# Kernel tuning notes

Measured on AMD Instinct MI355X. Metric: run time of the kernel, lower is better.

Reference implementation:

```python
import jax, jax.numpy as jnp
import numpy as np

B = 512              # number of graphs
NODES_PER_G = 256    # equal-size graphs (required by jagged reshape in original)
N = B * NODES_PER_G  # total nodes
DEG = 16
E = N * DEG
F = 16               # num_node_features (coords + 2-dim selected encoding)
D = 64               # embedding_dim
H = 128              # hidden_output_dim
A = 1                # actions_output_dim
MAX_LV = 3


def setup_inputs() -> dict:
    key = jax.random.key(0)
    ks = jax.random.split(key, 12)
    node_features = jax.random.normal(ks[0], (N, F), dtype=jnp.float32)
    # edges restricted to within each graph, fixed out-degree DEG
    edge_dst = jnp.repeat(jnp.arange(N, dtype=jnp.int32), DEG)
    base = (edge_dst // NODES_PER_G) * NODES_PER_G
    edge_src = base + jax.random.randint(ks[1], (E,), 0, NODES_PER_G, dtype=jnp.int32)
    seg_ids = (jnp.arange(N, dtype=jnp.int32) // NODES_PER_G)
    forbidden_mask = jax.random.bernoulli(ks[2], 0.1, (N,))
    s = 1.0 / np.sqrt(F)
    Wn = jax.random.uniform(ks[3], (F, D), jnp.float32, -s, s)
    bn = jax.random.uniform(ks[4], (D,), jnp.float32, -s, s)
    s = 1.0 / np.sqrt(D)
    Wc = jax.random.uniform(ks[5], (D, D), jnp.float32, -s, s)
    bc = jax.random.uniform(ks[6], (D,), jnp.float32, -s, s)
    s = 1.0 / np.sqrt(2 * D)
    W1 = jax.random.uniform(ks[7], (2 * D, H), jnp.float32, -s, s)
    b1 = jax.random.uniform(ks[8], (H,), jnp.float32, -s, s)
    s = 1.0 / np.sqrt(H)
    W2 = jax.random.uniform(ks[9], (H, A), jnp.float32, -s, s)
    b2 = jax.random.uniform(ks[10], (A,), jnp.float32, -s, s)
    return {"node_features": node_features, "edge_src": edge_src, "edge_dst": edge_dst,
            "seg_ids": seg_ids, "forbidden_mask": forbidden_mask,
            "Wn": Wn, "bn": bn, "Wc": Wc, "bc": bc,
            "W1": W1, "b1": b1, "W2": W2, "b2": b2}


def reference(node_features, edge_src, edge_dst, seg_ids, forbidden_mask,
              Wn, bn, Wc, bc, W1, b1, W2, b2):
    # --- structure2vec mean-field (EmbedMeanField, output_dim=0, max_lv=3) ---
    input_msg = node_features @ Wn + bn            # [N, D]
    h = jax.nn.relu(input_msg)
    for _ in range(MAX_LV):
        pooled = jax.ops.segment_sum(h[edge_src], edge_dst, num_segments=N)  # adjacency spmm
        h = jax.nn.relu(pooled @ Wc + bc + input_msg)
    graph_embed = jax.nn.relu(jax.ops.segment_sum(h, seg_ids, num_segments=B))  # [B, D]
    # --- actions is None: repeat graph embed per node, concat, small MLP ---
    rep = graph_embed[seg_ids]                     # rep_global_embed
    embed_s_a = jnp.concatenate([h, rep], axis=1)  # [N, 2D]
    raw_pred = jax.nn.relu(embed_s_a @ W1 + b1) @ W2 + b2  # [N, A]
    # --- greedy action select with forbidden-action masking + jagged topk ---
    q = raw_pred.reshape(-1)                       # A == 1
    q = jnp.where(forbidden_mask, jnp.float32(np.finfo(np.float32).min), q)
    jag = q.reshape(B, NODES_PER_G)
    values = jnp.max(jag, axis=1, keepdims=True)
    indices = jnp.argmax(jag, axis=1, keepdims=True)
    return indices, raw_pred, values
```

## Files before the change

### kernel.cpp

```cpp
#include <hip/hip_runtime.h>

#define NB 512
#define NPG 256
#define NTOT (NB * NPG)
#define NEGMIN -3.4028234663852886e38f

#define OFF_WNT 0
#define OFF_WCT 1024
#define OFF_W1AT 5120
#define OFF_W1BT 13312
#define OFF_BNC 21504
#define WS_FLOATS 21568

__global__ __launch_bounds__(256) void prep_kernel(
    const float* __restrict__ Wn, const float* __restrict__ bn,
    const float* __restrict__ Wc, const float* __restrict__ bc,
    const float* __restrict__ W1, float* __restrict__ ws)
{
    int i = blockIdx.x * 256 + threadIdx.x;
    if (i < 1024) {
        int d = i >> 4, k = i & 15;
        ws[OFF_WNT + i] = Wn[k * 64 + d];
    } else if (i < 5120) {
        int j = i - 1024; int d = j >> 6, k = j & 63;
        ws[OFF_WCT + j] = Wc[k * 64 + d];
    } else if (i < 13312) {
        int j = i - 5120; int r = j >> 6, k = j & 63;
        ws[OFF_W1AT + j] = W1[k * 128 + r];
    } else if (i < 21504) {
        int j = i - 13312; int r = j >> 6, k = j & 63;
        ws[OFF_W1BT + j] = W1[(64 + k) * 128 + r];
    } else if (i < WS_FLOATS) {
        int d = i - OFF_BNC;
        ws[OFF_BNC + d] = bn[d] + bc[d];
    }
}

__global__ __launch_bounds__(256, 2) void gdqn_kernel(
    const float* __restrict__ nfg, const int* __restrict__ esrcg,
    const int* __restrict__ fmask, const float* __restrict__ ws,
    const float* __restrict__ bn, const float* __restrict__ b1,
    const float* __restrict__ W2, const float* __restrict__ b2,
    float* __restrict__ out)
{
    extern __shared__ float smem[];
    float* hsh  = smem;
    float* part = smem + 16384;
    float* gesh = smem + 16640;
    float* rpsh = smem + 16704;
    float* redv = smem + 16832;
    int*   redi = (int*)(smem + 16836);

    const int g = blockIdx.x, t = threadIdx.x;
    const int node = (g << 8) + t;
    const int swt = t & 7;
    float* myrow = hsh + (t << 6);

    const float* WnT  = ws + OFF_WNT;
    const float* WcT  = ws + OFF_WCT;
    const float* W1aT = ws + OFF_W1AT;
    const float* bnc  = ws + OFF_BNC;

    float nf[16];
    {
        const float4* p = (const float4*)(nfg + node * 16);
        float4 a = p[0], b = p[1], c = p[2], d = p[3];
        nf[0]=a.x; nf[1]=a.y; nf[2]=a.z; nf[3]=a.w;
        nf[4]=b.x; nf[5]=b.y; nf[6]=b.z; nf[7]=b.w;
        nf[8]=c.x; nf[9]=c.y; nf[10]=c.z; nf[11]=c.w;
        nf[12]=d.x; nf[13]=d.y; nf[14]=d.z; nf[15]=d.w;
    }
    int es[16];
    {
        const int4* p = (const int4*)(esrcg + node * 16);
        int4 a = p[0], b = p[1], c = p[2], d = p[3];
        es[0]=a.x&255; es[1]=a.y&255; es[2]=a.z&255; es[3]=a.w&255;
        es[4]=b.x&255; es[5]=b.y&255; es[6]=b.z&255; es[7]=b.w&255;
        es[8]=c.x&255; es[9]=c.y&255; es[10]=c.z&255; es[11]=c.w&255;
        es[12]=d.x&255; es[13]=d.y&255; es[14]=d.z&255; es[15]=d.w&255;
    }

    for (int c = 0; c < 16; ++c) {
        float s4[4];
        #pragma unroll
        for (int q = 0; q < 4; ++q) {
            int d = 4 * c + q;
            float s = bn[d];
            #pragma unroll
            for (int k = 0; k < 16; ++k) s = fmaf(nf[k], WnT[d * 16 + k], s);
            s4[q] = fmaxf(s, 0.0f);
        }
        ((float4*)myrow)[c ^ swt] = make_float4(s4[0], s4[1], s4[2], s4[3]);
    }
    __syncthreads();

    for (int lv = 0; lv < 3; ++lv) {
        float pooled[64];
        #pragma unroll
        for (int k = 0; k < 64; ++k) pooled[k] = 0.0f;
        #pragma unroll
        for (int j = 0; j < 16; ++j) {
            int s = es[j];
            const float4* row = (const float4*)(hsh + (s << 6));
            int sw = s & 7;
            #pragma unroll
            for (int c = 0; c < 16; ++c) {
                float4 v = row[c ^ sw];
                pooled[4*c+0] += v.x; pooled[4*c+1] += v.y;
                pooled[4*c+2] += v.z; pooled[4*c+3] += v.w;
            }
        }
        __syncthreads();

        for (int c = 0; c < 16; ++c) {
            float s4[4];
            #pragma unroll
            for (int q = 0; q < 4; ++q) {
                int d = 4 * c + q;
                float s = bnc[d];
                #pragma unroll
                for (int k = 0; k < 16; ++k) s = fmaf(nf[k], WnT[d * 16 + k], s);
                const float* wr = WcT + d * 64;
                #pragma unroll
                for (int k = 0; k < 64; ++k) s = fmaf(pooled[k], wr[k], s);
                s4[q] = fmaxf(s, 0.0f);
            }
            ((float4*)myrow)[c ^ swt] = make_float4(s4[0], s4[1], s4[2], s4[3]);
        }
        __syncthreads();
    }

    {
        int col = t & 63, v0 = (t >> 6) << 6;
        float s = 0.0f;
        for (int v = 0; v < 64; ++v) {
            int vv = v0 + v;
            s += hsh[(vv << 6) + ((((col >> 2) ^ (vv & 7)) << 2) | (col & 3))];
        }
        part[t] = s;
    }
    __syncthreads();
    if (t < 64) {
        float s = part[t] + part[t + 64] + part[t + 128] + part[t + 192];
        gesh[t] = fmaxf(s, 0.0f);
    }
    __syncthreads();
    if (t < 128) {
        float s = b1[t];
        const float4* wr = (const float4*)(ws + OFF_W1BT + t * 64);
        #pragma unroll
        for (int c = 0; c < 16; ++c) {
            float4 w = wr[c];
            s = fmaf(gesh[4*c+0], w.x, s);
            s = fmaf(gesh[4*c+1], w.y, s);
            s = fmaf(gesh[4*c+2], w.z, s);
            s = fmaf(gesh[4*c+3], w.w, s);
        }
        rpsh[t] = s;
    }

    float h[64];
    #pragma unroll
    for (int c = 0; c < 16; ++c) {
        float4 v = ((const float4*)myrow)[c ^ swt];
        h[4*c+0] = v.x; h[4*c+1] = v.y; h[4*c+2] = v.z; h[4*c+3] = v.w;
    }
    __syncthreads();

    float raw = b2[0];
    for (int j = 0; j < 128; ++j) {
        float z = rpsh[j];
        const float* wr = W1aT + j * 64;
        #pragma unroll
        for (int k = 0; k < 64; ++k) z = fmaf(h[k], wr[k], z);
        raw = fmaf(fmaxf(z, 0.0f), W2[j], raw);
    }
    out[512 + node] = raw;

    float q = fmask[node] ? NEGMIN : raw;
    int idx = t;
    #pragma unroll
    for (int off = 32; off >= 1; off >>= 1) {
        float ov = __shfl_down(q, off, 64);
        int oi  = __shfl_down(idx, off, 64);
        if (ov > q || (ov == q && oi < idx)) { q = ov; idx = oi; }
    }
    if ((t & 63) == 0) { redv[t >> 6] = q; redi[t >> 6] = idx; }
    __syncthreads();
    if (t == 0) {
        float bv = redv[0]; int bi = redi[0];
        #pragma unroll
        for (int w = 1; w < 4; ++w) {
            float v = redv[w]; int iw = redi[w];
            if (v > bv || (v == bv && iw < bi)) { bv = v; bi = iw; }
        }
        out[g] = (float)bi;
        out[512 + NTOT + g] = bv;
    }
}

extern "C" void kernel_launch(void* const* d_in, const int* in_sizes, int n_in,
                              void* d_out, int out_size, void* d_ws, size_t ws_size,
                              hipStream_t stream)
{
    const float* nfg   = (const float*)d_in[0];
    const int*   esrc  = (const int*)d_in[1];
    const int*   fmask = (const int*)d_in[4];
    const float* Wn = (const float*)d_in[5];
    const float* bn = (const float*)d_in[6];
    const float* Wc = (const float*)d_in[7];
    const float* bc = (const float*)d_in[8];
    const float* W1 = (const float*)d_in[9];
    const float* b1 = (const float*)d_in[10];
    const float* W2 = (const float*)d_in[11];
    const float* b2 = (const float*)d_in[12];
    float* out = (float*)d_out;
    float* ws  = (float*)d_ws;

    prep_kernel<<<(WS_FLOATS + 255) / 256, 256, 0, stream>>>(Wn, bn, Wc, bc, W1, ws);

    size_t shmem = 16840 * sizeof(float);
    hipFuncSetAttribute((const void*)gdqn_kernel,
                        hipFuncAttributeMaxDynamicSharedMemorySize, (int)shmem);
    gdqn_kernel<<<NB, 256, shmem, stream>>>(nfg, esrc, fmask, ws, bn, b1, W2, b2, out);
}
```

Before: 260.8 us.

## Split each node's feature dimension across two threads with 512-thread blocks

The kernel now launches 512 threads per graph, and each node is handled by two threads that each own half of the 64 embedding columns. The edge-gather aggregation and the Wc matvec are split by column half. Pooled rows are exchanged through shared memory using extra barriers. The per-node input message (nf·Wn + bn + bc) is computed once and kept in registers instead of being recomputed every level, and edge indices are packed into bytes to save registers. This raises parallelism and occupancy for the message-passing phase, at the cost of more syncthreads and half the threads idling in the MLP head.

```diff
diff --git a/kernel.cpp b/kernel.cpp
--- a/kernel.cpp
+++ b/kernel.cpp
@@ -36,7 +36,7 @@
     }
 }
 
-__global__ __launch_bounds__(256, 2) void gdqn_kernel(
+__global__ __launch_bounds__(512, 4) void gdqn_kernel(
     const float* __restrict__ nfg, const int* __restrict__ esrcg,
     const int* __restrict__ fmask, const float* __restrict__ ws,
     const float* __restrict__ bn, const float* __restrict__ b1,
@@ -52,9 +52,11 @@
     int*   redi = (int*)(smem + 16836);
 
     const int g = blockIdx.x, t = threadIdx.x;
-    const int node = (g << 8) + t;
-    const int swt = t & 7;
-    float* myrow = hsh + (t << 6);
+    const int n = t & 255;
+    const int H = __builtin_amdgcn_readfirstlane(t >> 8);
+    const int node = (g << 8) + n;
+    const int sw = n & 7;
+    float* myrow = hsh + (n << 6);
 
     const float* WnT  = ws + OFF_WNT;
     const float* WcT  = ws + OFF_WCT;
@@ -70,67 +72,89 @@
         nf[8]=c.x; nf[9]=c.y; nf[10]=c.z; nf[11]=c.w;
         nf[12]=d.x; nf[13]=d.y; nf[14]=d.z; nf[15]=d.w;
     }
-    int es[16];
+    int esp[4];
     {
         const int4* p = (const int4*)(esrcg + node * 16);
         int4 a = p[0], b = p[1], c = p[2], d = p[3];
-        es[0]=a.x&255; es[1]=a.y&255; es[2]=a.z&255; es[3]=a.w&255;
-        es[4]=b.x&255; es[5]=b.y&255; es[6]=b.z&255; es[7]=b.w&255;
-        es[8]=c.x&255; es[9]=c.y&255; es[10]=c.z&255; es[11]=c.w&255;
-        es[12]=d.x&255; es[13]=d.y&255; es[14]=d.z&255; es[15]=d.w&255;
-    }
-
-    for (int c = 0; c < 16; ++c) {
+        esp[0] = (a.x&255) | ((a.y&255)<<8) | ((a.z&255)<<16) | ((a.w&255)<<24);
+        esp[1] = (b.x&255) | ((b.y&255)<<8) | ((b.z&255)<<16) | ((b.w&255)<<24);
+        esp[2] = (c.x&255) | ((c.y&255)<<8) | ((c.z&255)<<16) | ((c.w&255)<<24);
+        esp[3] = (d.x&255) | ((d.y&255)<<8) | ((d.z&255)<<16) | ((d.w&255)<<24);
+    }
+
+    const int dbase = H << 5;
+    float imc[32];
+    #pragma unroll
+    for (int c = 0; c < 8; ++c) {
         float s4[4];
         #pragma unroll
         for (int q = 0; q < 4; ++q) {
-            int d = 4 * c + q;
-            float s = bn[d];
-            #pragma unroll
-            for (int k = 0; k < 16; ++k) s = fmaf(nf[k], WnT[d * 16 + k], s);
-            s4[q] = fmaxf(s, 0.0f);
-        }
-        ((float4*)myrow)[c ^ swt] = make_float4(s4[0], s4[1], s4[2], s4[3]);
-    }
-    __syncthreads();
-
+            int dq = 4 * c + q, d = dbase + dq;
+            float s0 = bn[d], si = bnc[d];
+            #pragma unroll
+            for (int k = 0; k < 16; ++k) {
+                float w = WnT[d * 16 + k];
+                s0 = fmaf(nf[k], w, s0);
+                si = fmaf(nf[k], w, si);
+            }
+            imc[dq] = si;
+            s4[q] = fmaxf(s0, 0.0f);
+        }
+        ((float4*)myrow)[((H << 3) | c) ^ sw] = make_float4(s4[0], s4[1], s4[2], s4[3]);
+    }
+    __syncthreads();
+
+    const int Hb = H << 7;
     for (int lv = 0; lv < 3; ++lv) {
-        float pooled[64];
-        #pragma unroll
-        for (int k = 0; k < 64; ++k) pooled[k] = 0.0f;
+        float own[32];
+        #pragma unroll
+        for (int i = 0; i < 32; ++i) own[i] = 0.0f;
+        const char* bp = (const char*)hsh;
         #pragma unroll
         for (int j = 0; j < 16; ++j) {
-            int s = es[j];
-            const float4* row = (const float4*)(hsh + (s << 6));
-            int sw = s & 7;
-            #pragma unroll
-            for (int c = 0; c < 16; ++c) {
-                float4 v = row[c ^ sw];
-                pooled[4*c+0] += v.x; pooled[4*c+1] += v.y;
-                pooled[4*c+2] += v.z; pooled[4*c+3] += v.w;
+            int s = (esp[j >> 2] >> ((j & 3) * 8)) & 255;
+            int vb = (s << 8) | ((s & 7) << 4) | Hb;
+            #pragma unroll
+            for (int c = 0; c < 8; ++c) {
+                float4 v = *(const float4*)(bp + (vb ^ (c << 4)));
+                own[4*c+0] += v.x; own[4*c+1] += v.y;
+                own[4*c+2] += v.z; own[4*c+3] += v.w;
             }
         }
         __syncthreads();
 
+        #pragma unroll
+        for (int c = 0; c < 8; ++c)
+            ((float4*)myrow)[((H << 3) | c) ^ sw] =
+                make_float4(own[4*c+0], own[4*c+1], own[4*c+2], own[4*c+3]);
+        __syncthreads();
+
+        float pl[64];
+        #pragma unroll
         for (int c = 0; c < 16; ++c) {
+            float4 v = ((const float4*)myrow)[c ^ sw];
+            pl[4*c+0] = v.x; pl[4*c+1] = v.y; pl[4*c+2] = v.z; pl[4*c+3] = v.w;
+        }
+        __syncthreads();
+
+        #pragma unroll
+        for (int c = 0; c < 8; ++c) {
             float s4[4];
             #pragma unroll
             for (int q = 0; q < 4; ++q) {
-                int d = 4 * c + q;
-                float s = bnc[d];
+                int dq = 4 * c + q, d = dbase + dq;
+                const float* wr = WcT + d * 64;
+                float s = imc[dq];
                 #pragma unroll
-                for (int k = 0; k < 16; ++k) s = fmaf(nf[k], WnT[d * 16 + k], s);
-                const float* wr = WcT + d * 64;
-                #pragma unroll
-                for (int k = 0; k < 64; ++k) s = fmaf(pooled[k], wr[k], s);
+                for (int k = 0; k < 64; ++k) s = fmaf(pl[k], wr[k], s);
                 s4[q] = fmaxf(s, 0.0f);
             }
-            ((float4*)myrow)[c ^ swt] = make_float4(s4[0], s4[1], s4[2], s4[3]);
-        }
-        __syncthreads();
-    }
-
-    {
+            ((float4*)myrow)[((H << 3) | c) ^ sw] = make_float4(s4[0], s4[1], s4[2], s4[3]);
+        }
+        __syncthreads();
+    }
+
+    if (t < 256) {
         int col = t & 63, v0 = (t >> 6) << 6;
         float s = 0.0f;
         for (int v = 0; v < 64; ++v) {
@@ -158,34 +182,36 @@
         }
         rpsh[t] = s;
     }
-
-    float h[64];
-    #pragma unroll
-    for (int c = 0; c < 16; ++c) {
-        float4 v = ((const float4*)myrow)[c ^ swt];
-        h[4*c+0] = v.x; h[4*c+1] = v.y; h[4*c+2] = v.z; h[4*c+3] = v.w;
-    }
-    __syncthreads();
-
-    float raw = b2[0];
-    for (int j = 0; j < 128; ++j) {
-        float z = rpsh[j];
-        const float* wr = W1aT + j * 64;
-        #pragma unroll
-        for (int k = 0; k < 64; ++k) z = fmaf(h[k], wr[k], z);
-        raw = fmaf(fmaxf(z, 0.0f), W2[j], raw);
-    }
-    out[512 + node] = raw;
-
-    float q = fmask[node] ? NEGMIN : raw;
-    int idx = t;
-    #pragma unroll
-    for (int off = 32; off >= 1; off >>= 1) {
-        float ov = __shfl_down(q, off, 64);
-        int oi  = __shfl_down(idx, off, 64);
-        if (ov > q || (ov == q && oi < idx)) { q = ov; idx = oi; }
-    }
-    if ((t & 63) == 0) { redv[t >> 6] = q; redi[t >> 6] = idx; }
+    __syncthreads();
+
+    if (t < 256) {
+        float h[64];
+        #pragma unroll
+        for (int c = 0; c < 16; ++c) {
+            float4 v = ((const float4*)myrow)[c ^ sw];
+            h[4*c+0] = v.x; h[4*c+1] = v.y; h[4*c+2] = v.z; h[4*c+3] = v.w;
+        }
+
+        float raw = b2[0];
+        for (int j = 0; j < 128; ++j) {
+            float z = rpsh[j];
+            const float* wr = W1aT + j * 64;
+            #pragma unroll
+            for (int k = 0; k < 64; ++k) z = fmaf(h[k], wr[k], z);
+            raw = fmaf(fmaxf(z, 0.0f), W2[j], raw);
+        }
+        out[512 + node] = raw;
+
+        float q = fmask[node] ? NEGMIN : raw;
+        int idx = t;
+        #pragma unroll
+        for (int off = 32; off >= 1; off >>= 1) {
+            float ov = __shfl_down(q, off, 64);
+            int oi  = __shfl_down(idx, off, 64);
+            if (ov > q || (ov == q && oi < idx)) { q = ov; idx = oi; }
+        }
+        if ((t & 63) == 0) { redv[t >> 6] = q; redi[t >> 6] = idx; }
+    }
     __syncthreads();
     if (t == 0) {
         float bv = redv[0]; int bi = redi[0];
@@ -222,5 +248,5 @@
     size_t shmem = 16840 * sizeof(float);
     hipFuncSetAttribute((const void*)gdqn_kernel,
                         hipFuncAttributeMaxDynamicSharedMemorySize, (int)shmem);
-    gdqn_kernel<<<NB, 256, shmem, stream>>>(nfg, esrc, fmask, ws, bn, b1, W2, b2, out);
+    gdqn_kernel<<<NB, 512, shmem, stream>>>(nfg, esrc, fmask, ws, bn, b1, W2, b2, out);
 }
```

Result: slower. 361.2 us (+38.5%).
